# Optimization experiments

Measured on AMD Instinct MI355X. Metric: run time of the kernel, lower is better.

The kernel has to match this reference:

```python
import jax, jax.numpy as jnp
import numpy as np

N_NODES = 50000
N_EDGES = 1600000
IN_CH = 128
OUT_CH = 128
MAX_NORM = 1.0


def setup_inputs() -> dict:
    key = jax.random.key(0)
    k1, k2, k3, k4 = jax.random.split(key, 4)
    x = jax.random.normal(k1, (N_NODES, IN_CH), dtype=jnp.float32)
    edge_index = jax.random.randint(k2, (2, N_EDGES), 0, N_NODES, dtype=jnp.int64)
    # GCNConv lin: weight [out, in] (kaiming-ish init), bias [out] zeros-ish
    W = jax.random.normal(k3, (OUT_CH, IN_CH), dtype=jnp.float32) * (1.0 / np.sqrt(IN_CH))
    b = jax.random.normal(k4, (OUT_CH,), dtype=jnp.float32) * 0.01
    return {"x": x, "edge_index": edge_index, "W": W, "b": b}


def _renorm_cols(W, max_norm):
    # torch.renorm(W, p=2, dim=1, maxnorm): each slice along dim 1 (column of [out,in])
    # is rescaled so its L2 norm <= max_norm.
    norms = jnp.sqrt(jnp.sum(W * W, axis=0, keepdims=True))  # [1, in]
    scale = jnp.where(norms > max_norm, max_norm / norms, 1.0)
    return W * scale


def reference(x, edge_index, W, b):
    N = x.shape[0]
    Wn = _renorm_cols(W, MAX_NORM)
    # Linear transform first (as PyG GCNConv does): h = x @ W^T
    h = jnp.einsum('ni,oi->no', x, Wn)  # [N, out]

    # Add self loops
    row = jnp.concatenate([edge_index[0], jnp.arange(N, dtype=edge_index.dtype)])
    col = jnp.concatenate([edge_index[1], jnp.arange(N, dtype=edge_index.dtype)])

    # Symmetric normalization: deg over destination (col), edge weights = 1
    ones = jnp.ones(row.shape[0], dtype=h.dtype)
    deg = jax.ops.segment_sum(ones, col, num_segments=N)
    deg_inv_sqrt = jnp.where(deg > 0, jax.lax.rsqrt(deg), 0.0)
    norm = deg_inv_sqrt[row] * deg_inv_sqrt[col]  # [E+N]

    # Gather source features, scale, scatter-add to destinations
    msgs = h[row] * norm[:, None]  # [E+N, out]
    out = jax.ops.segment_sum(msgs, col, num_segments=N)
    return out + b
```

## Files before the change

kernel.cpp:

```cpp
#include <hip/hip_runtime.h>

#define N_NODES 50000
#define N_EDGES 1600000
#define CH 128
#define NB 196
#define CHUNK_E 2048
#define NCHUNK 782
#define GEMMB 782
#define CAP 12288

#define WS_CURSOR  0
#define WS_ROWPTR  1024
#define WS_DINV    201728
#define WS_SCL     401728
#define WS_SRC     601728
#define WS_Q8      7001728
#define WS_BINS    13401728

typedef __bf16 bf16x8 __attribute__((ext_vector_type(8)));
typedef float f32x4 __attribute__((ext_vector_type(4)));

__device__ __forceinline__ unsigned int pack_bf16(float a, float b) {
    unsigned int ua = __builtin_bit_cast(unsigned int, a);
    unsigned int ub = __builtin_bit_cast(unsigned int, b);
    ua = (ua + 0x7FFFu + ((ua >> 16) & 1u)) >> 16;
    ub = (ub + 0x7FFFu + ((ub >> 16) & 1u)) >> 16;
    return ua | (ub << 16);
}

__global__ __launch_bounds__(256) void k_fused(const float* __restrict__ x,
                                               const float* __restrict__ W,
                                               const int* __restrict__ eidx,
                                               int* __restrict__ cursor,
                                               unsigned int* __restrict__ bins,
                                               unsigned int* __restrict__ q8,
                                               float* __restrict__ scl) {
    __shared__ uint4 SMEM[3072];
    __shared__ float s_scale[128];
    __shared__ float s_part[256];
    __shared__ int s_st;
    int t = threadIdx.x;

    if (blockIdx.x < NCHUNK) {
        int c = blockIdx.x;
        int* lc    = (int*)SMEM;
        int* lbase = (int*)SMEM + 256;
        unsigned int* stash = (unsigned int*)SMEM + 512;
        lc[t] = 0;
        if (t < 64) {
            int v = eidx[2 * t + 1];
            unsigned long long m = __ballot(v == 0);
            if (t == 0) s_st = (m == ~0ull) ? 2 : 1;
        }
        __syncthreads();
        int st = s_st;
        long base = (long)c * CHUNK_E;
        #pragma unroll
        for (int i = 0; i < 4; ++i) {
            long e0 = base + (long)(i * 256 + t) * 2;
            unsigned int u0 = 0xFFFFFFFFu, u1 = 0xFFFFFFFFu;
            if (e0 < N_EDGES) {
                unsigned int r0, r1, c0, c1;
                if (st == 2) {
                    uint4 rw = *(const uint4*)&eidx[2 * e0];
                    uint4 cw = *(const uint4*)&eidx[2 * (N_EDGES + e0)];
                    r0 = rw.x; r1 = rw.z; c0 = cw.x; c1 = cw.z;
                } else {
                    uint2 rw = *(const uint2*)&eidx[e0];
                    uint2 cw = *(const uint2*)&eidx[N_EDGES + e0];
                    r0 = rw.x; r1 = rw.y; c0 = cw.x; c1 = cw.y;
                }
                u0 = r0 | (c0 << 16);
                u1 = r1 | (c1 << 16);
                atomicAdd(&lc[c0 >> 8], 1);
                atomicAdd(&lc[c1 >> 8], 1);
            }
            stash[i * 512 + 2 * t]     = u0;
            stash[i * 512 + 2 * t + 1] = u1;
        }
        __syncthreads();
        if (t < NB && lc[t] > 0) lbase[t] = atomicAdd(&cursor[t], lc[t]);
        __syncthreads();
        #pragma unroll
        for (int i = 0; i < 8; ++i) {
            unsigned int u = stash[i * 256 + t];
            if (u != 0xFFFFFFFFu) {
                int bb = u >> 24;
                int pos = atomicAdd(&lbase[bb], 1);
                bins[(size_t)bb * CAP + pos] = (u & 0xFFFFu) | (((u >> 16) & 0xFFu) << 16);
            }
        }
        return;
    }

    uint4* xs = SMEM;
    uint4* wsl = SMEM + 1024;
    float* scratch = (float*)SMEM;
    int base = (blockIdx.x - NCHUNK) * 64;
    {
        int ct = t & 127, oh = (t >> 7) * 64;
        float s = 0.f;
        #pragma unroll 8
        for (int o = 0; o < 64; ++o) {
            float w = W[(size_t)(oh + o) * CH + ct];
            s += w * w;
        }
        s_part[t] = s;
        __syncthreads();
        if (t < 128) {
            float tot = s_part[t] + s_part[t + 128];
            s_scale[t] = (tot > 1.0f) ? rsqrtf(tot) : 1.0f;
        }
    }
    #pragma unroll
    for (int it = 0; it < 4; ++it) {
        int idx = it * 256 + t;
        int r = idx >> 4, c16 = idx & 15;
        int n = base + r;
        float4 v0 = make_float4(0.f, 0.f, 0.f, 0.f), v1 = v0;
        if (n < N_NODES) {
            v0 = *(const float4*)&x[(size_t)n * CH + c16 * 8];
            v1 = *(const float4*)&x[(size_t)n * CH + c16 * 8 + 4];
        }
        uint4 p;
        p.x = pack_bf16(v0.x, v0.y); p.y = pack_bf16(v0.z, v0.w);
        p.z = pack_bf16(v1.x, v1.y); p.w = pack_bf16(v1.z, v1.w);
        xs[r * 16 + (c16 ^ (r & 7))] = p;
    }
    __syncthreads();
    #pragma unroll
    for (int it = 0; it < 8; ++it) {
        int idx = it * 256 + t;
        int o = idx >> 4, c16 = idx & 15;
        float4 v0 = *(const float4*)&W[(size_t)o * CH + c16 * 8];
        float4 v1 = *(const float4*)&W[(size_t)o * CH + c16 * 8 + 4];
        int k0 = c16 * 8;
        v0.x *= s_scale[k0];     v0.y *= s_scale[k0 + 1];
        v0.z *= s_scale[k0 + 2]; v0.w *= s_scale[k0 + 3];
        v1.x *= s_scale[k0 + 4]; v1.y *= s_scale[k0 + 5];
        v1.z *= s_scale[k0 + 6]; v1.w *= s_scale[k0 + 7];
        uint4 p;
        p.x = pack_bf16(v0.x, v0.y); p.y = pack_bf16(v0.z, v0.w);
        p.z = pack_bf16(v1.x, v1.y); p.w = pack_bf16(v1.z, v1.w);
        wsl[o * 16 + (c16 ^ (o & 7))] = p;
    }
    __syncthreads();
    int w = t >> 6, l = t & 63;
    int lrow = w * 16 + (l & 15);
    int hi = l >> 4;
    bf16x8 a[4];
    #pragma unroll
    for (int ks = 0; ks < 4; ++ks) {
        int c16 = ks * 4 + hi;
        a[ks] = __builtin_bit_cast(bf16x8, xs[lrow * 16 + (c16 ^ (lrow & 7))]);
    }
    float vals[8][4];
    #pragma unroll
    for (int tc = 0; tc < 8; ++tc) {
        int col = tc * 16 + (l & 15);
        f32x4 acc = {0.f, 0.f, 0.f, 0.f};
        #pragma unroll
        for (int ks = 0; ks < 4; ++ks) {
            int c16 = ks * 4 + hi;
            bf16x8 bf = __builtin_bit_cast(bf16x8, wsl[col * 16 + (c16 ^ (col & 7))]);
            acc = __builtin_amdgcn_mfma_f32_16x16x32_bf16(a[ks], bf, acc, 0, 0, 0);
        }
        #pragma unroll
        for (int r = 0; r < 4; ++r) vals[tc][r] = acc[r];
    }
    __syncthreads();
    #pragma unroll
    for (int tc = 0; tc < 8; ++tc) {
        int col = tc * 16 + (l & 15);
        #pragma unroll
        for (int r = 0; r < 4; ++r) {
            int rl = w * 16 + hi * 4 + r;
            scratch[rl * 132 + col] = vals[tc][r];
        }
    }
    __syncthreads();
    int rl = t >> 2, q = t & 3;
    const float4* rp = (const float4*)&scratch[rl * 132 + q * 32];
    float4 f[8];
    float m = 0.f;
    #pragma unroll
    for (int k = 0; k < 8; ++k) {
        f[k] = rp[k];
        m = fmaxf(m, fmaxf(fmaxf(fabsf(f[k].x), fabsf(f[k].y)),
                           fmaxf(fabsf(f[k].z), fabsf(f[k].w))));
    }
    m = fmaxf(m, __shfl_xor(m, 1));
    m = fmaxf(m, __shfl_xor(m, 2));
    float sc = m * (1.0f / 127.0f);
    float inv = (m > 0.f) ? (127.0f / m) : 0.f;
    int n = base + rl;
    if (n < N_NODES) {
        unsigned int u[8];
        #pragma unroll
        for (int k = 0; k < 8; ++k) {
            int b0 = __float2int_rn(f[k].x * inv) + 128;
            int b1 = __float2int_rn(f[k].y * inv) + 128;
            int b2 = __float2int_rn(f[k].z * inv) + 128;
            int b3 = __float2int_rn(f[k].w * inv) + 128;
            u[k] = (unsigned int)b0 | ((unsigned int)b1 << 8) |
                   ((unsigned int)b2 << 16) | ((unsigned int)b3 << 24);
        }
        uint4* qp = (uint4*)&q8[(size_t)n * 32 + q * 8];
        qp[0] = make_uint4(u[0], u[1], u[2], u[3]);
        qp[1] = make_uint4(u[4], u[5], u[6], u[7]);
        if (q == 0) scl[n] = sc;
    }
}

__global__ __launch_bounds__(256) void k_sort(const unsigned int* __restrict__ bins,
                                              const int* __restrict__ cursor,
                                              int* __restrict__ rowptr,
                                              float* __restrict__ dinv,
                                              float* __restrict__ scl,
                                              int* __restrict__ src) {
    __shared__ int shA[256], shB[256], shC[256];
    __shared__ int s_g0, s_sz;
    int t = threadIdx.x, b = blockIdx.x;
    int v = (t < NB) ? cursor[t] : 0;
    shC[t] = v;
    __syncthreads();
    for (int off = 1; off < 256; off <<= 1) {
        int u = (t >= off) ? shC[t - off] : 0;
        __syncthreads();
        shC[t] += u;
        __syncthreads();
    }
    if (t == b) { s_g0 = shC[t] - v; s_sz = v; }
    __syncthreads();
    int g0 = s_g0, sz = s_sz;
    const unsigned int* reg = bins + (size_t)b * CAP;
    shA[t] = 0;
    __syncthreads();
    for (int i = t; i < sz; i += 256) {
        unsigned int p = reg[i];
        atomicAdd(&shA[(p >> 16) & 255], 1);
    }
    __syncthreads();
    int d = shA[t];
    shC[t] = d;
    __syncthreads();
    for (int off = 1; off < 256; off <<= 1) {
        int u = (t >= off) ? shC[t - off] : 0;
        __syncthreads();
        shC[t] += u;
        __syncthreads();
    }
    int local_rp = g0 + shC[t] - d;
    int n = (b << 8) + t;
    if (n < N_NODES) {
        rowptr[n] = local_rp;
        float dv = rsqrtf((float)(d + 1));
        dinv[n] = dv;
        scl[n] *= dv;
    }
    if (b == NB - 1 && t == 0) rowptr[N_NODES] = N_EDGES;
    shB[t] = local_rp;
    __syncthreads();
    for (int i = t; i < sz; i += 256) {
        unsigned int p = reg[i];
        int pos = atomicAdd(&shB[(p >> 16) & 255], 1);
        src[pos] = (int)(p & 0xFFFFu);
    }
}

__global__ __launch_bounds__(256) void k_gather(const int* __restrict__ rowptr,
                                                const int* __restrict__ src,
                                                const unsigned int* __restrict__ q8,
                                                const float* __restrict__ scl,
                                                const float* __restrict__ dinv,
                                                const float* __restrict__ b,
                                                float* __restrict__ out) {
    int t = threadIdx.x;
    int wid = t >> 6, lane = t & 63;
    int half = lane >> 5, lc = lane & 31;
    int n = blockIdx.x * 4 + wid;
    if (n >= N_NODES) return;
    int j0 = rowptr[n], j1 = rowptr[n + 1];
    float a0 = 0.f, a1 = 0.f, a2 = 0.f, a3 = 0.f, asum = 0.f;
    int jj = j0;
    for (; jj + 32 <= j1; jj += 32) {
        int rs[16];
        #pragma unroll
        for (int k = 0; k < 16; ++k) rs[k] = src[jj + 2 * k + half];
        float ss[16];
        unsigned int vs[16];
        #pragma unroll
        for (int k = 0; k < 16; ++k) {
            ss[k] = scl[rs[k]];
            vs[k] = q8[((unsigned)rs[k] << 5) + lc];
        }
        #pragma unroll
        for (int k = 0; k < 16; ++k) {
            a0 = fmaf((float)(vs[k] & 0xFFu), ss[k], a0);
            a1 = fmaf((float)((vs[k] >> 8) & 0xFFu), ss[k], a1);
            a2 = fmaf((float)((vs[k] >> 16) & 0xFFu), ss[k], a2);
            a3 = fmaf((float)(vs[k] >> 24), ss[k], a3);
            asum += ss[k];
        }
    }
    for (; jj + 8 <= j1; jj += 8) {
        int rs[4];
        #pragma unroll
        for (int k = 0; k < 4; ++k) rs[k] = src[jj + 2 * k + half];
        #pragma unroll
        for (int k = 0; k < 4; ++k) {
            float sc = scl[rs[k]];
            unsigned int v = q8[((unsigned)rs[k] << 5) + lc];
            a0 = fmaf((float)(v & 0xFFu), sc, a0);
            a1 = fmaf((float)((v >> 8) & 0xFFu), sc, a1);
            a2 = fmaf((float)((v >> 16) & 0xFFu), sc, a2);
            a3 = fmaf((float)(v >> 24), sc, a3);
            asum += sc;
        }
    }
    for (; jj + 2 <= j1; jj += 2) {
        int r = src[jj + half];
        float sc = scl[r];
        unsigned int v = q8[((unsigned)r << 5) + lc];
        a0 = fmaf((float)(v & 0xFFu), sc, a0);
        a1 = fmaf((float)((v >> 8) & 0xFFu), sc, a1);
        a2 = fmaf((float)((v >> 16) & 0xFFu), sc, a2);
        a3 = fmaf((float)(v >> 24), sc, a3);
        asum += sc;
    }
    if (jj < j1 && half == 0) {
        int r = src[jj];
        float sc = scl[r];
        unsigned int v = q8[((unsigned)r << 5) + lc];
        a0 = fmaf((float)(v & 0xFFu), sc, a0);
        a1 = fmaf((float)((v >> 8) & 0xFFu), sc, a1);
        a2 = fmaf((float)((v >> 16) & 0xFFu), sc, a2);
        a3 = fmaf((float)(v >> 24), sc, a3);
        asum += sc;
    }
    a0 += __shfl_xor(a0, 32);
    a1 += __shfl_xor(a1, 32);
    a2 += __shfl_xor(a2, 32);
    a3 += __shfl_xor(a3, 32);
    asum += __shfl_xor(asum, 32);
    if (half == 0) {
        float di = dinv[n];
        float sc = scl[n];
        unsigned int v = q8[((unsigned)n << 5) + lc];
        float4 bv = *(const float4*)&b[4 * lc];
        float bias128 = 128.0f * asum;
        float s0 = (float)(v & 0xFFu) - 128.0f;
        float s1 = (float)((v >> 8) & 0xFFu) - 128.0f;
        float s2 = (float)((v >> 16) & 0xFFu) - 128.0f;
        float s3 = (float)(v >> 24) - 128.0f;
        float4 o;
        o.x = (a0 - bias128 + s0 * sc) * di + bv.x;
        o.y = (a1 - bias128 + s1 * sc) * di + bv.y;
        o.z = (a2 - bias128 + s2 * sc) * di + bv.z;
        o.w = (a3 - bias128 + s3 * sc) * di + bv.w;
        *(float4*)&out[(size_t)n * CH + 4 * lc] = o;
    }
}

extern "C" void kernel_launch(void* const* d_in, const int* in_sizes, int n_in,
                              void* d_out, int out_size, void* d_ws, size_t ws_size,
                              hipStream_t stream) {
    const float* x = (const float*)d_in[0];
    const int* eidx = (const int*)d_in[1];
    const float* W = (const float*)d_in[2];
    const float* b = (const float*)d_in[3];
    float* out = (float*)d_out;

    char* ws = (char*)d_ws;
    int*   cursor        = (int*)(ws + WS_CURSOR);
    int*   rowptr        = (int*)(ws + WS_ROWPTR);
    float* dinv          = (float*)(ws + WS_DINV);
    float* sclp          = (float*)(ws + WS_SCL);
    int*   srcarr        = (int*)(ws + WS_SRC);
    unsigned int* q8     = (unsigned int*)(ws + WS_Q8);
    unsigned int* bins   = (unsigned int*)(ws + WS_BINS);

    hipMemsetAsync(cursor, 0, NB * sizeof(int), stream);
    k_fused<<<NCHUNK + GEMMB, 256, 0, stream>>>(x, W, eidx, cursor, bins, q8, sclp);
    k_sort<<<NB, 256, 0, stream>>>(bins, cursor, rowptr, dinv, sclp, srcarr);
    k_gather<<<(N_NODES + 3) / 4, 256, 0, stream>>>(rowptr, srcarr, q8, sclp, dinv, b, out);
}
```

Measured before the change: 116.2 us.

## Store per-edge source scale alongside index and use persistent gather blocks

The sort kernel is split in two so that the second pass can read the finalized per-node scale and write (src, scale) pairs into the CSR array. The gather then reads the scale with the index instead of doing a dependent random load of scl[src]. The gather also becomes grid-stride over 2048 blocks with a smaller 16-edge unroll. This costs an extra kernel launch, another pass over the bins, and a CSR array twice as large.

```diff
diff --git a/kernel.cpp b/kernel.cpp
--- a/kernel.cpp
+++ b/kernel.cpp
@@ -8,14 +8,15 @@
 #define NCHUNK 782
 #define GEMMB 782
 #define CAP 12288
+#define GATHB 2048
 
 #define WS_CURSOR  0
 #define WS_ROWPTR  1024
 #define WS_DINV    201728
 #define WS_SCL     401728
-#define WS_SRC     601728
-#define WS_Q8      7001728
-#define WS_BINS    13401728
+#define WS_Q8      601728
+#define WS_SRC2    7001728
+#define WS_BINS    19801728
 
 typedef __bf16 bf16x8 __attribute__((ext_vector_type(8)));
 typedef float f32x4 __attribute__((ext_vector_type(4)));
@@ -212,13 +213,12 @@
     }
 }
 
-__global__ __launch_bounds__(256) void k_sort(const unsigned int* __restrict__ bins,
-                                              const int* __restrict__ cursor,
-                                              int* __restrict__ rowptr,
-                                              float* __restrict__ dinv,
-                                              float* __restrict__ scl,
-                                              int* __restrict__ src) {
-    __shared__ int shA[256], shB[256], shC[256];
+__global__ __launch_bounds__(256) void k_sortA(const unsigned int* __restrict__ bins,
+                                               const int* __restrict__ cursor,
+                                               int* __restrict__ rowptr,
+                                               float* __restrict__ dinv,
+                                               float* __restrict__ scl) {
+    __shared__ int shA[256], shC[256];
     __shared__ int s_g0, s_sz;
     int t = threadIdx.x, b = blockIdx.x;
     int v = (t < NB) ? cursor[t] : 0;
@@ -259,17 +259,34 @@
         scl[n] *= dv;
     }
     if (b == NB - 1 && t == 0) rowptr[N_NODES] = N_EDGES;
-    shB[t] = local_rp;
-    __syncthreads();
+}
+
+__global__ __launch_bounds__(256) void k_sortB(const unsigned int* __restrict__ bins,
+                                               const int* __restrict__ cursor,
+                                               const int* __restrict__ rowptr,
+                                               const float* __restrict__ scl,
+                                               uint2* __restrict__ src2) {
+    __shared__ int shB[256], shC[256];
+    __shared__ int s_sz;
+    int t = threadIdx.x, b = blockIdx.x;
+    if (t == 0) s_sz = cursor[b];
+    int n = (b << 8) + t;
+    shB[t] = (n < N_NODES) ? rowptr[n] : 0;
+    __syncthreads();
+    int sz = s_sz;
+    const unsigned int* reg = bins + (size_t)b * CAP;
     for (int i = t; i < sz; i += 256) {
         unsigned int p = reg[i];
+        int row = (int)(p & 0xFFFFu);
         int pos = atomicAdd(&shB[(p >> 16) & 255], 1);
-        src[pos] = (int)(p & 0xFFFFu);
-    }
+        src2[pos] = make_uint2((unsigned int)row,
+                               __builtin_bit_cast(unsigned int, scl[row]));
+    }
+    (void)shC;
 }
 
 __global__ __launch_bounds__(256) void k_gather(const int* __restrict__ rowptr,
-                                                const int* __restrict__ src,
+                                                const uint2* __restrict__ src2,
                                                 const unsigned int* __restrict__ q8,
                                                 const float* __restrict__ scl,
                                                 const float* __restrict__ dinv,
@@ -278,87 +295,69 @@
     int t = threadIdx.x;
     int wid = t >> 6, lane = t & 63;
     int half = lane >> 5, lc = lane & 31;
-    int n = blockIdx.x * 4 + wid;
-    if (n >= N_NODES) return;
-    int j0 = rowptr[n], j1 = rowptr[n + 1];
-    float a0 = 0.f, a1 = 0.f, a2 = 0.f, a3 = 0.f, asum = 0.f;
-    int jj = j0;
-    for (; jj + 32 <= j1; jj += 32) {
-        int rs[16];
-        #pragma unroll
-        for (int k = 0; k < 16; ++k) rs[k] = src[jj + 2 * k + half];
-        float ss[16];
-        unsigned int vs[16];
-        #pragma unroll
-        for (int k = 0; k < 16; ++k) {
-            ss[k] = scl[rs[k]];
-            vs[k] = q8[((unsigned)rs[k] << 5) + lc];
-        }
-        #pragma unroll
-        for (int k = 0; k < 16; ++k) {
-            a0 = fmaf((float)(vs[k] & 0xFFu), ss[k], a0);
-            a1 = fmaf((float)((vs[k] >> 8) & 0xFFu), ss[k], a1);
-            a2 = fmaf((float)((vs[k] >> 16) & 0xFFu), ss[k], a2);
-            a3 = fmaf((float)(vs[k] >> 24), ss[k], a3);
-            asum += ss[k];
-        }
-    }
-    for (; jj + 8 <= j1; jj += 8) {
-        int rs[4];
-        #pragma unroll
-        for (int k = 0; k < 4; ++k) rs[k] = src[jj + 2 * k + half];
-        #pragma unroll
-        for (int k = 0; k < 4; ++k) {
-            float sc = scl[rs[k]];
-            unsigned int v = q8[((unsigned)rs[k] << 5) + lc];
+    for (int n = blockIdx.x * 4 + wid; n < N_NODES; n += GATHB * 4) {
+        int j0 = rowptr[n], j1 = rowptr[n + 1];
+        float a0 = 0.f, a1 = 0.f, a2 = 0.f, a3 = 0.f, asum = 0.f;
+        int jj = j0;
+        for (; jj + 16 <= j1; jj += 16) {
+            uint2 rs[8];
+            #pragma unroll
+            for (int k = 0; k < 8; ++k) rs[k] = src2[jj + 2 * k + half];
+            unsigned int vs[8];
+            #pragma unroll
+            for (int k = 0; k < 8; ++k) vs[k] = q8[((size_t)rs[k].x << 5) + lc];
+            #pragma unroll
+            for (int k = 0; k < 8; ++k) {
+                float sc = __builtin_bit_cast(float, rs[k].y);
+                a0 = fmaf((float)(vs[k] & 0xFFu), sc, a0);
+                a1 = fmaf((float)((vs[k] >> 8) & 0xFFu), sc, a1);
+                a2 = fmaf((float)((vs[k] >> 16) & 0xFFu), sc, a2);
+                a3 = fmaf((float)(vs[k] >> 24), sc, a3);
+                asum += sc;
+            }
+        }
+        for (; jj + 2 <= j1; jj += 2) {
+            uint2 r = src2[jj + half];
+            float sc = __builtin_bit_cast(float, r.y);
+            unsigned int v = q8[((size_t)r.x << 5) + lc];
             a0 = fmaf((float)(v & 0xFFu), sc, a0);
             a1 = fmaf((float)((v >> 8) & 0xFFu), sc, a1);
             a2 = fmaf((float)((v >> 16) & 0xFFu), sc, a2);
             a3 = fmaf((float)(v >> 24), sc, a3);
             asum += sc;
         }
-    }
-    for (; jj + 2 <= j1; jj += 2) {
-        int r = src[jj + half];
-        float sc = scl[r];
-        unsigned int v = q8[((unsigned)r << 5) + lc];
-        a0 = fmaf((float)(v & 0xFFu), sc, a0);
-        a1 = fmaf((float)((v >> 8) & 0xFFu), sc, a1);
-        a2 = fmaf((float)((v >> 16) & 0xFFu), sc, a2);
-        a3 = fmaf((float)(v >> 24), sc, a3);
-        asum += sc;
-    }
-    if (jj < j1 && half == 0) {
-        int r = src[jj];
-        float sc = scl[r];
-        unsigned int v = q8[((unsigned)r << 5) + lc];
-        a0 = fmaf((float)(v & 0xFFu), sc, a0);
-        a1 = fmaf((float)((v >> 8) & 0xFFu), sc, a1);
-        a2 = fmaf((float)((v >> 16) & 0xFFu), sc, a2);
-        a3 = fmaf((float)(v >> 24), sc, a3);
-        asum += sc;
-    }
-    a0 += __shfl_xor(a0, 32);
-    a1 += __shfl_xor(a1, 32);
-    a2 += __shfl_xor(a2, 32);
-    a3 += __shfl_xor(a3, 32);
-    asum += __shfl_xor(asum, 32);
-    if (half == 0) {
-        float di = dinv[n];
-        float sc = scl[n];
-        unsigned int v = q8[((unsigned)n << 5) + lc];
-        float4 bv = *(const float4*)&b[4 * lc];
-        float bias128 = 128.0f * asum;
-        float s0 = (float)(v & 0xFFu) - 128.0f;
-        float s1 = (float)((v >> 8) & 0xFFu) - 128.0f;
-        float s2 = (float)((v >> 16) & 0xFFu) - 128.0f;
-        float s3 = (float)(v >> 24) - 128.0f;
-        float4 o;
-        o.x = (a0 - bias128 + s0 * sc) * di + bv.x;
-        o.y = (a1 - bias128 + s1 * sc) * di + bv.y;
-        o.z = (a2 - bias128 + s2 * sc) * di + bv.z;
-        o.w = (a3 - bias128 + s3 * sc) * di + bv.w;
-        *(float4*)&out[(size_t)n * CH + 4 * lc] = o;
+        if (jj < j1 && half == 0) {
+            uint2 r = src2[jj];
+            float sc = __builtin_bit_cast(float, r.y);
+            unsigned int v = q8[((size_t)r.x << 5) + lc];
+            a0 = fmaf((float)(v & 0xFFu), sc, a0);
+            a1 = fmaf((float)((v >> 8) & 0xFFu), sc, a1);
+            a2 = fmaf((float)((v >> 16) & 0xFFu), sc, a2);
+            a3 = fmaf((float)(v >> 24), sc, a3);
+            asum += sc;
+        }
+        a0 += __shfl_xor(a0, 32);
+        a1 += __shfl_xor(a1, 32);
+        a2 += __shfl_xor(a2, 32);
+        a3 += __shfl_xor(a3, 32);
+        asum += __shfl_xor(asum, 32);
+        if (half == 0) {
+            float di = dinv[n];
+            float sc = scl[n];
+            unsigned int v = q8[((size_t)n << 5) + lc];
+            float4 bv = *(const float4*)&b[4 * lc];
+            float bias128 = 128.0f * asum;
+            float s0 = (float)(v & 0xFFu) - 128.0f;
+            float s1 = (float)((v >> 8) & 0xFFu) - 128.0f;
+            float s2 = (float)((v >> 16) & 0xFFu) - 128.0f;
+            float s3 = (float)(v >> 24) - 128.0f;
+            float4 o;
+            o.x = (a0 - bias128 + s0 * sc) * di + bv.x;
+            o.y = (a1 - bias128 + s1 * sc) * di + bv.y;
+            o.z = (a2 - bias128 + s2 * sc) * di + bv.z;
+            o.w = (a3 - bias128 + s3 * sc) * di + bv.w;
+            *(float4*)&out[(size_t)n * CH + 4 * lc] = o;
+        }
     }
 }
 
@@ -376,12 +375,13 @@
     int*   rowptr        = (int*)(ws + WS_ROWPTR);
     float* dinv          = (float*)(ws + WS_DINV);
     float* sclp          = (float*)(ws + WS_SCL);
-    int*   srcarr        = (int*)(ws + WS_SRC);
     unsigned int* q8     = (unsigned int*)(ws + WS_Q8);
+    uint2* src2          = (uint2*)(ws + WS_SRC2);
     unsigned int* bins   = (unsigned int*)(ws + WS_BINS);
 
     hipMemsetAsync(cursor, 0, NB * sizeof(int), stream);
     k_fused<<<NCHUNK + GEMMB, 256, 0, stream>>>(x, W, eidx, cursor, bins, q8, sclp);
-    k_sort<<<NB, 256, 0, stream>>>(bins, cursor, rowptr, dinv, sclp, srcarr);
-    k_gather<<<(N_NODES + 3) / 4, 256, 0, stream>>>(rowptr, srcarr, q8, sclp, dinv, b, out);
-}
+    k_sortA<<<NB, 256, 0, stream>>>(bins, cursor, rowptr, dinv, sclp);
+    k_sortB<<<NB, 256, 0, stream>>>(bins, cursor, rowptr, sclp, src2);
+    k_gather<<<GATHB, 256, 0, stream>>>(rowptr, src2, q8, sclp, dinv, b, out);
+}
```

After: 123.2 us. 6.0% more time.
